# Performance work log

Measured on AMD Instinct MI355X. Metric: run time of the kernel, lower is better.

The kernel has to match this reference:

```python
import jax, jax.numpy as jnp
import numpy as np

EPS = 1e-5

def layer_norm(x, g, b):
    mu = jnp.mean(x, axis=-1, keepdims=True)
    var = jnp.mean(jnp.square(x - mu), axis=-1, keepdims=True)
    return (x - mu) * jax.lax.rsqrt(var + EPS) * g + b

def setup_inputs() -> dict:
    key = jax.random.key(0)
    ks = jax.random.split(key, 12)
    I, H, N = 512, 512, 65536
    s = 0.02
    return {
        "x": jax.random.normal(ks[0], (I,), dtype=jnp.float32),
        "hiddens": jax.random.normal(ks[1], (N, H), dtype=jnp.float32),
        "Wz": jax.random.normal(ks[2], (H, I + H), dtype=jnp.float32) * s,
        "Wri": jax.random.normal(ks[3], (H, I), dtype=jnp.float32) * s,
        "Wrh": jax.random.normal(ks[4], (H, H), dtype=jnp.float32) * s,
        "Wu": jax.random.normal(ks[5], (H, I + H), dtype=jnp.float32) * s,
        "gz": jnp.ones((H,), jnp.float32), "bz": jnp.zeros((H,), jnp.float32),
        "gr": jnp.ones((H,), jnp.float32), "br": jnp.zeros((H,), jnp.float32),
        "gu": jnp.ones((H,), jnp.float32), "bu": jnp.zeros((H,), jnp.float32),
    }

def reference(x, hiddens, Wz, Wri, Wrh, Wu, gz, bz, gr, br, gu, bu):
    # hiddens: [N, H] stacked child hidden states; x: [I]
    hidden_sum = hiddens.sum(0)  # [H]
    # r gate: per-child linear + LayerNorm + sigmoid -> [N, H]
    r_pre = x @ Wri.T + hiddens @ Wrh.T  # broadcast input term over children
    r = jax.nn.sigmoid(layer_norm(r_pre, gr, br))
    # z gate over (input, sum of child hiddens)
    z = jax.nn.sigmoid(layer_norm(jnp.concatenate([x, hidden_sum]) @ Wz.T, gz, bz))
    # candidate with reset-gated child sum
    u = jnp.tanh(layer_norm(jnp.concatenate([x, (r * hiddens).sum(0)]) @ Wu.T, gu, bu))
    h = z * hidden_sum + (1.0 - z) * u
    return h
```

## Files before the change

kernel.cpp:

```cpp
#include <hip/hip_runtime.h>

#define HDIM 512
#define BM 128

typedef __attribute__((ext_vector_type(8))) short bf16x8;
typedef __attribute__((ext_vector_type(4))) float f32x4;

__device__ __forceinline__ unsigned short f2bf(float f){
  union { float f; unsigned int u; } c; c.f = f;
  unsigned int u = c.u;
  unsigned int r = u + 0x7fffu + ((u >> 16) & 1u);
  return (unsigned short)(r >> 16);
}
__device__ __forceinline__ float bf2f(unsigned short b){
  union { unsigned int u; float f; } c; c.u = ((unsigned int)b) << 16;
  return c.f;
}
__device__ __forceinline__ unsigned int pack_trunc(float a, float b){
  return __builtin_amdgcn_perm(__float_as_uint(b), __float_as_uint(a), 0x07060302u);
}
template<int CTRL>
__device__ __forceinline__ float dpp_add(float x){
  int y = __builtin_amdgcn_update_dpp(0, __float_as_int(x), CTRL, 0xf, 0xf, true);
  return x + __int_as_float(y);
}
__device__ __forceinline__ float row_sum16(float x){
  x = dpp_add<0xB1>(x);
  x = dpp_add<0x4E>(x);
  x = dpp_add<0x124>(x);
  x = dpp_add<0x128>(x);
  return x;
}

__global__ __launch_bounds__(256) void prep_k(const float* __restrict__ Wrh,
    unsigned short* __restrict__ wpack, const float* __restrict__ Wri,
    const float* __restrict__ x, float* __restrict__ xwri)
{
  int b = blockIdx.x;
  if (b < 128){
    int t    = b * 256 + threadIdx.x;
    int lane = t & 63;
    int g    = t >> 6;
    int ni   = g & 3;
    int kkk  = (g >> 2) & 15;
    int wc   = g >> 6;
    int row  = wc * 64 + ni * 16 + (lane & 15);
    int k0   = kkk * 32 + (lane >> 4) * 8;
    const float* src = Wrh + (size_t)row * HDIM + k0;
    float4 f0 = *(const float4*)(src);
    float4 f1 = *(const float4*)(src + 4);
    bf16x8 v;
    v[0]=(short)f2bf(f0.x); v[1]=(short)f2bf(f0.y); v[2]=(short)f2bf(f0.z); v[3]=(short)f2bf(f0.w);
    v[4]=(short)f2bf(f1.x); v[5]=(short)f2bf(f1.y); v[6]=(short)f2bf(f1.z); v[7]=(short)f2bf(f1.w);
    *(bf16x8*)(wpack + (size_t)t * 8) = v;
  } else {
    int lane = threadIdx.x & 63, wid = threadIdx.x >> 6;
    int row = (b - 128) * 4 + wid;
    const float* Wr = Wri + (size_t)row * HDIM;
    float a = 0.f;
    #pragma unroll
    for (int k = 0; k < HDIM / 64; k++) a += x[k*64 + lane] * Wr[k*64 + lane];
    #pragma unroll
    for (int m = 1; m < 64; m <<= 1) a += __shfl_xor(a, m, 64);
    if (lane == 0) xwri[row] = a;
  }
}

__global__ __launch_bounds__(1024, 4) void fused_r(
    const float* __restrict__ hiddens,
    const unsigned short* __restrict__ wpack,
    const float* __restrict__ xWri,
    const float* __restrict__ gr, const float* __restrict__ br,
    float* __restrict__ psum_rh, float* __restrict__ psum_h)
{
  __shared__ short As[BM * HDIM];
  __shared__ float redS[8 * 128];
  __shared__ float redQ[8 * 128];
  __shared__ float mu_s[128], rs_s[128];

  const int tid    = threadIdx.x;
  const int lane   = tid & 63;
  const int wid    = tid >> 6;
  const int rowgrp = wid >> 3;
  const int colgrp = wid & 7;
  const int llo    = lane & 15;
  const int lhi    = lane >> 4;
  const int wcol   = colgrp * 64;
  const int rbase  = rowgrp * 64;
  const int r0     = blockIdx.x * BM;

  const int srow = tid >> 3;
  const int scs  = tid & 7;
  const float* aglob = hiddens + (size_t)(r0 + srow) * HDIM + scs * 8;
  char* const wptr = (char*)As + srow * 128 + ((scs * 16) ^ ((srow & 7) << 4));

  const int rdoff = (rbase + llo) * 128 + ((lhi * 16) ^ ((llo & 7) << 4));

  f32x4 acc[4][4];
  #pragma unroll
  for (int i = 0; i < 4; i++)
    #pragma unroll
    for (int j = 0; j < 4; j++)
      #pragma unroll
      for (int k = 0; k < 4; k++) acc[i][j][k] = 0.f;

  const bf16x8* wp = (const bf16x8*)wpack + ((size_t)colgrp * 64) * 64 + lane;
  {
    float4 f0 = *(const float4*)(aglob);
    float4 f1 = *(const float4*)(aglob + 4);
    uint4 w;
    w.x = pack_trunc(f0.x, f0.y); w.y = pack_trunc(f0.z, f0.w);
    w.z = pack_trunc(f1.x, f1.y); w.w = pack_trunc(f1.z, f1.w);
    *(uint4*)(wptr) = w;
  }
  float4 pA0 = *(const float4*)(aglob + 64);
  float4 pA1 = *(const float4*)(aglob + 68);
  asm volatile("s_waitcnt lgkmcnt(0)" ::: "memory");
  __builtin_amdgcn_s_barrier();

  #pragma unroll 1
  for (int p = 0; p < 8; p++){
    const int pb = p * 16384;
    bf16x8 bfr[4];
    #pragma unroll
    for (int ni = 0; ni < 4; ni++) bfr[ni] = wp[(2 * p) * 256 + ni * 64];
    bf16x8 af[4];
    #pragma unroll
    for (int mi = 0; mi < 4; mi++)
      af[mi] = *(const bf16x8*)((char*)As + (pb + rdoff + mi * 2048));
    if (p < 7){
      uint4 w;
      w.x = pack_trunc(pA0.x, pA0.y); w.y = pack_trunc(pA0.z, pA0.w);
      w.z = pack_trunc(pA1.x, pA1.y); w.w = pack_trunc(pA1.z, pA1.w);
      *(uint4*)(wptr + (p + 1) * 16384) = w;
    }
    if (p < 6){
      pA0 = *(const float4*)(aglob + (p + 2) * 64);
      pA1 = *(const float4*)(aglob + (p + 2) * 64 + 4);
    }
    __builtin_amdgcn_s_setprio(1);
    #pragma unroll
    for (int mi = 0; mi < 4; mi++)
      #pragma unroll
      for (int ni = 0; ni < 4; ni++)
        acc[mi][ni] = __builtin_amdgcn_mfma_f32_16x16x32_bf16(af[mi], bfr[ni], acc[mi][ni], 0, 0, 0);
    __builtin_amdgcn_s_setprio(0);
    #pragma unroll
    for (int ni = 0; ni < 4; ni++) bfr[ni] = wp[(2 * p + 1) * 256 + ni * 64];
    #pragma unroll
    for (int mi = 0; mi < 4; mi++)
      af[mi] = *(const bf16x8*)((char*)As + ((pb + rdoff + mi * 2048) ^ 64));
    __builtin_amdgcn_s_setprio(1);
    #pragma unroll
    for (int mi = 0; mi < 4; mi++)
      #pragma unroll
      for (int ni = 0; ni < 4; ni++)
        acc[mi][ni] = __builtin_amdgcn_mfma_f32_16x16x32_bf16(af[mi], bfr[ni], acc[mi][ni], 0, 0, 0);
    __builtin_amdgcn_s_setprio(0);
    asm volatile("s_waitcnt lgkmcnt(0)" ::: "memory");
    __builtin_amdgcn_s_barrier();
  }

  float xw[4], g4[4], b4[4];
  #pragma unroll
  for (int ni = 0; ni < 4; ni++){
    int c = wcol + ni * 16 + llo;
    xw[ni] = xWri[c];
    g4[ni] = gr[c];
    b4[ni] = br[c];
  }
  #pragma unroll
  for (int mi = 0; mi < 4; mi++){
    #pragma unroll
    for (int rr = 0; rr < 4; rr++){
      float sv = 0.f, qv = 0.f;
      #pragma unroll
      for (int ni = 0; ni < 4; ni++){
        float v = acc[mi][ni][rr] + xw[ni];
        acc[mi][ni][rr] = v;
        sv += v; qv += v * v;
      }
      sv = row_sum16(sv);
      qv = row_sum16(qv);
      if (llo == 0){
        int row = rbase + mi * 16 + lhi * 4 + rr;
        redS[colgrp * 128 + row] = sv;
        redQ[colgrp * 128 + row] = qv;
      }
    }
  }
  __syncthreads();
  if (tid < 128){
    float S = 0.f, Q = 0.f;
    #pragma unroll
    for (int w = 0; w < 8; w++){ S += redS[w * 128 + tid]; Q += redQ[w * 128 + tid]; }
    float mu  = S * (1.f / 512.f);
    float var = Q * (1.f / 512.f) - mu * mu;
    mu_s[tid] = mu;
    rs_s[tid] = rsqrtf(var + 1e-5f);
  }
  __syncthreads();

  float prh[4] = {0.f, 0.f, 0.f, 0.f};
  float ph [4] = {0.f, 0.f, 0.f, 0.f};
  #pragma unroll
  for (int mi = 0; mi < 4; mi++){
    #pragma unroll
    for (int rr = 0; rr < 4; rr++){
      int row = rbase + mi * 16 + lhi * 4 + rr;
      float mu = mu_s[row], rs = rs_s[row];
      int sw2 = (row & 7) << 4;
      #pragma unroll
      for (int ni = 0; ni < 4; ni++){
        float v = (acc[mi][ni][rr] - mu) * rs * g4[ni] + b4[ni];
        float r = __builtin_amdgcn_rcpf(1.f + __expf(-v));
        int cb = ni * 32 + llo * 2;
        float h = bf2f(*(const unsigned short*)((char*)As + colgrp * 16384
                     + row * 128 + (cb ^ sw2)));
        prh[ni] += r * h;
        ph [ni] += h;
      }
    }
  }
  #pragma unroll
  for (int ni = 0; ni < 4; ni++){
    prh[ni] += __shfl_xor(prh[ni], 16, 64);
    prh[ni] += __shfl_xor(prh[ni], 32, 64);
    ph [ni] += __shfl_xor(ph [ni], 16, 64);
    ph [ni] += __shfl_xor(ph [ni], 32, 64);
  }
  float* ppRH = redS;
  float* ppH  = redQ;
  if (lhi == 0){
    #pragma unroll
    for (int ni = 0; ni < 4; ni++){
      int col = wcol + ni * 16 + llo;
      ppRH[rowgrp * 512 + col] = prh[ni];
      ppH [rowgrp * 512 + col] = ph[ni];
    }
  }
  __syncthreads();
  if (tid < 512){
    psum_rh[(size_t)blockIdx.x * HDIM + tid] = ppRH[tid] + ppRH[512 + tid];
    psum_h [(size_t)blockIdx.x * HDIM + tid] = ppH[tid]  + ppH[512 + tid];
  }
}

__global__ __launch_bounds__(256) void reduce_psums(
    const float* __restrict__ psum_rh, const float* __restrict__ psum_h,
    const float* __restrict__ x, float* __restrict__ catz, float* __restrict__ catu,
    int nblk)
{
  __shared__ float L[8][32];
  int b = blockIdx.x, t = threadIdx.x;
  if (b < 32){
    const float* P = (b < 16) ? psum_rh : psum_h;
    int c0 = (b & 15) * 32;
    int wj = t >> 5, ci = t & 31;
    float a = 0.f;
    for (int s = wj; s < nblk; s += 8) a += P[(size_t)s * 512 + c0 + ci];
    L[wj][ci] = a;
    __syncthreads();
    if (t < 32){
      float r = 0.f;
      #pragma unroll
      for (int w = 0; w < 8; w++) r += L[w][t];
      if (b < 16) catu[512 + c0 + t] = r;
      else        catz[512 + c0 + t] = r;
    }
  } else {
    int i = ((b - 32) & 1) * 256 + t;
    if (b < 34) catz[i] = x[i];
    else        catu[i] = x[i];
  }
}

__global__ __launch_bounds__(256) void matvec_zu(
    const float* __restrict__ Wz, const float* __restrict__ Wu,
    const float* __restrict__ catz, const float* __restrict__ catu,
    float* __restrict__ zpre, float* __restrict__ upre)
{
  int b = blockIdx.x, lane = threadIdx.x & 63, wid = threadIdx.x >> 6;
  int row = (b & 127) * 4 + wid;
  const float* W = (b < 128) ? Wz : Wu;
  const float* v = (b < 128) ? catz : catu;
  float*       o = (b < 128) ? zpre : upre;
  const float* Wr = W + (size_t)row * 1024;
  float a = 0.f;
  #pragma unroll
  for (int k = 0; k < 1024 / 64; k++) a += v[k*64 + lane] * Wr[k*64 + lane];
  #pragma unroll
  for (int m = 1; m < 64; m <<= 1) a += __shfl_xor(a, m, 64);
  if (lane == 0) o[row] = a;
}

__global__ __launch_bounds__(512) void finalize_k(
    const float* __restrict__ zpre, const float* __restrict__ upre,
    const float* __restrict__ gz, const float* __restrict__ bz,
    const float* __restrict__ gu, const float* __restrict__ bu,
    const float* __restrict__ catz, float* __restrict__ out)
{
  __shared__ float R[8][4];
  int t = threadIdx.x, lane = t & 63, wid = t >> 6;
  float zp = zpre[t], up = upre[t];
  float zs = zp, zq = zp * zp, us = up, uq = up * up;
  #pragma unroll
  for (int m = 1; m < 64; m <<= 1){
    zs += __shfl_xor(zs, m, 64); zq += __shfl_xor(zq, m, 64);
    us += __shfl_xor(us, m, 64); uq += __shfl_xor(uq, m, 64);
  }
  if (lane == 0){ R[wid][0] = zs; R[wid][1] = zq; R[wid][2] = us; R[wid][3] = uq; }
  __syncthreads();
  float ZS = 0.f, ZQ = 0.f, US = 0.f, UQ = 0.f;
  #pragma unroll
  for (int w = 0; w < 8; w++){ ZS += R[w][0]; ZQ += R[w][1]; US += R[w][2]; UQ += R[w][3]; }
  float zmu = ZS / 512.f, zrs = rsqrtf(ZQ / 512.f - zmu * zmu + 1e-5f);
  float umu = US / 512.f, urs = rsqrtf(UQ / 512.f - umu * umu + 1e-5f);
  float z = 1.f / (1.f + expf(-((zp - zmu) * zrs * gz[t] + bz[t])));
  float u = tanhf((up - umu) * urs * gu[t] + bu[t]);
  float hs = catz[512 + t];
  out[t] = z * hs + (1.f - z) * u;
}

extern "C" void kernel_launch(void* const* d_in, const int* in_sizes, int n_in,
                              void* d_out, int out_size, void* d_ws, size_t ws_size,
                              hipStream_t stream)
{
  const float* x   = (const float*)d_in[0];
  const float* hid = (const float*)d_in[1];
  const float* Wz  = (const float*)d_in[2];
  const float* Wri = (const float*)d_in[3];
  const float* Wrh = (const float*)d_in[4];
  const float* Wu  = (const float*)d_in[5];
  const float* gz  = (const float*)d_in[6];
  const float* bz  = (const float*)d_in[7];
  const float* gr  = (const float*)d_in[8];
  const float* br  = (const float*)d_in[9];
  const float* gu  = (const float*)d_in[10];
  const float* bu  = (const float*)d_in[11];
  (void)n_in; (void)out_size; (void)ws_size;

  const int M    = in_sizes[1] / HDIM;
  const int nblk = M / BM;

  char* ws = (char*)d_ws;
  unsigned short* wpack = (unsigned short*)ws;
  float* xwri    = (float*)(ws + 524288);
  float* psum_rh = (float*)(ws + 526336);
  float* psum_h  = (float*)(ws + 526336 + (size_t)nblk * 2048);
  char*  p2      = ws + 526336 + (size_t)nblk * 4096;
  float* catz    = (float*)p2;
  float* catu    = (float*)(p2 + 4096);
  float* zpre    = (float*)(p2 + 8192);
  float* upre    = (float*)(p2 + 10240);
  float* out     = (float*)d_out;

  hipLaunchKernelGGL(prep_k,       dim3(256),  dim3(256),  0, stream, Wrh, wpack, Wri, x, xwri);
  hipLaunchKernelGGL(fused_r,      dim3(nblk), dim3(1024), 0, stream, hid, wpack, xwri, gr, br, psum_rh, psum_h);
  hipLaunchKernelGGL(reduce_psums, dim3(36),   dim3(256),  0, stream, psum_rh, psum_h, x, catz, catu, nblk);
  hipLaunchKernelGGL(matvec_zu,    dim3(256),  dim3(256),  0, stream, Wz, Wu, catz, catu, zpre, upre);
  hipLaunchKernelGGL(finalize_k,   dim3(1),    dim3(512),  0, stream, zpre, upre, gz, bz, gu, bu, catz, out);
}
```

Baseline: 89.70 us.

## Give each wave all 128 rows by 32 columns instead of a 64x64 tile

```diff
diff --git a/kernel.cpp b/kernel.cpp
--- a/kernel.cpp
+++ b/kernel.cpp
@@ -41,11 +41,11 @@
     int t    = b * 256 + threadIdx.x;
     int lane = t & 63;
     int g    = t >> 6;
-    int ni   = g & 3;
-    int kkk  = (g >> 2) & 15;
-    int wc   = g >> 6;
-    int row  = wc * 64 + ni * 16 + (lane & 15);
-    int k0   = kkk * 32 + (lane >> 4) * 8;
+    int ni   = g & 1;
+    int ks   = (g >> 1) & 15;
+    int wc   = g >> 5;
+    int row  = wc * 32 + ni * 16 + (lane & 15);
+    int k0   = ks * 32 + (lane >> 4) * 8;
     const float* src = Wrh + (size_t)row * HDIM + k0;
     float4 f0 = *(const float4*)(src);
     float4 f1 = *(const float4*)(src + 4);
@@ -74,19 +74,16 @@
     float* __restrict__ psum_rh, float* __restrict__ psum_h)
 {
   __shared__ short As[BM * HDIM];
-  __shared__ float redS[8 * 128];
-  __shared__ float redQ[8 * 128];
+  __shared__ float redS[16 * 128];
+  __shared__ float redQ[16 * 128];
   __shared__ float mu_s[128], rs_s[128];
 
   const int tid    = threadIdx.x;
   const int lane   = tid & 63;
-  const int wid    = tid >> 6;
-  const int rowgrp = wid >> 3;
-  const int colgrp = wid & 7;
+  const int colgrp = tid >> 6;
   const int llo    = lane & 15;
   const int lhi    = lane >> 4;
-  const int wcol   = colgrp * 64;
-  const int rbase  = rowgrp * 64;
+  const int wcol   = colgrp * 32;
   const int r0     = blockIdx.x * BM;
 
   const int srow = tid >> 3;
@@ -94,17 +91,17 @@
   const float* aglob = hiddens + (size_t)(r0 + srow) * HDIM + scs * 8;
   char* const wptr = (char*)As + srow * 128 + ((scs * 16) ^ ((srow & 7) << 4));
 
-  const int rdoff = (rbase + llo) * 128 + ((lhi * 16) ^ ((llo & 7) << 4));
-
-  f32x4 acc[4][4];
-  #pragma unroll
-  for (int i = 0; i < 4; i++)
-    #pragma unroll
-    for (int j = 0; j < 4; j++)
+  const int rdoff = llo * 128 + ((lhi * 16) ^ ((llo & 7) << 4));
+
+  f32x4 acc[8][2];
+  #pragma unroll
+  for (int i = 0; i < 8; i++)
+    #pragma unroll
+    for (int j = 0; j < 2; j++)
       #pragma unroll
       for (int k = 0; k < 4; k++) acc[i][j][k] = 0.f;
 
-  const bf16x8* wp = (const bf16x8*)wpack + ((size_t)colgrp * 64) * 64 + lane;
+  const bf16x8* wp = (const bf16x8*)wpack + ((size_t)colgrp * 32) * 64 + lane;
   {
     float4 f0 = *(const float4*)(aglob);
     float4 f1 = *(const float4*)(aglob + 4);
@@ -121,13 +118,6 @@
   #pragma unroll 1
   for (int p = 0; p < 8; p++){
     const int pb = p * 16384;
-    bf16x8 bfr[4];
-    #pragma unroll
-    for (int ni = 0; ni < 4; ni++) bfr[ni] = wp[(2 * p) * 256 + ni * 64];
-    bf16x8 af[4];
-    #pragma unroll
-    for (int mi = 0; mi < 4; mi++)
-      af[mi] = *(const bf16x8*)((char*)As + (pb + rdoff + mi * 2048));
     if (p < 7){
       uint4 w;
       w.x = pack_trunc(pA0.x, pA0.y); w.y = pack_trunc(pA0.z, pA0.w);
@@ -138,52 +128,59 @@
       pA0 = *(const float4*)(aglob + (p + 2) * 64);
       pA1 = *(const float4*)(aglob + (p + 2) * 64 + 4);
     }
-    __builtin_amdgcn_s_setprio(1);
-    #pragma unroll
-    for (int mi = 0; mi < 4; mi++)
-      #pragma unroll
-      for (int ni = 0; ni < 4; ni++)
-        acc[mi][ni] = __builtin_amdgcn_mfma_f32_16x16x32_bf16(af[mi], bfr[ni], acc[mi][ni], 0, 0, 0);
-    __builtin_amdgcn_s_setprio(0);
-    #pragma unroll
-    for (int ni = 0; ni < 4; ni++) bfr[ni] = wp[(2 * p + 1) * 256 + ni * 64];
-    #pragma unroll
-    for (int mi = 0; mi < 4; mi++)
-      af[mi] = *(const bf16x8*)((char*)As + ((pb + rdoff + mi * 2048) ^ 64));
-    __builtin_amdgcn_s_setprio(1);
-    #pragma unroll
-    for (int mi = 0; mi < 4; mi++)
-      #pragma unroll
-      for (int ni = 0; ni < 4; ni++)
-        acc[mi][ni] = __builtin_amdgcn_mfma_f32_16x16x32_bf16(af[mi], bfr[ni], acc[mi][ni], 0, 0, 0);
-    __builtin_amdgcn_s_setprio(0);
+    #pragma unroll
+    for (int kk = 0; kk < 2; kk++){
+      const int ksl = 2 * p + kk;
+      const int xo  = kk ? 64 : 0;
+      bf16x8 bfr[2];
+      #pragma unroll
+      for (int ni = 0; ni < 2; ni++) bfr[ni] = wp[(2 * ksl + ni) * 64];
+      bf16x8 af[4];
+      #pragma unroll
+      for (int mi = 0; mi < 4; mi++)
+        af[mi] = *(const bf16x8*)((char*)As + ((pb + rdoff + mi * 2048) ^ xo));
+      __builtin_amdgcn_s_setprio(1);
+      #pragma unroll
+      for (int mi = 0; mi < 4; mi++)
+        #pragma unroll
+        for (int ni = 0; ni < 2; ni++)
+          acc[mi][ni] = __builtin_amdgcn_mfma_f32_16x16x32_bf16(af[mi], bfr[ni], acc[mi][ni], 0, 0, 0);
+      __builtin_amdgcn_s_setprio(0);
+      #pragma unroll
+      for (int mi = 0; mi < 4; mi++)
+        af[mi] = *(const bf16x8*)((char*)As + ((pb + rdoff + (mi + 4) * 2048) ^ xo));
+      __builtin_amdgcn_s_setprio(1);
+      #pragma unroll
+      for (int mi = 0; mi < 4; mi++)
+        #pragma unroll
+        for (int ni = 0; ni < 2; ni++)
+          acc[mi + 4][ni] = __builtin_amdgcn_mfma_f32_16x16x32_bf16(af[mi], bfr[ni], acc[mi + 4][ni], 0, 0, 0);
+      __builtin_amdgcn_s_setprio(0);
+    }
     asm volatile("s_waitcnt lgkmcnt(0)" ::: "memory");
     __builtin_amdgcn_s_barrier();
   }
 
-  float xw[4], g4[4], b4[4];
-  #pragma unroll
-  for (int ni = 0; ni < 4; ni++){
+  float xw[2], g4[2], b4[2];
+  #pragma unroll
+  for (int ni = 0; ni < 2; ni++){
     int c = wcol + ni * 16 + llo;
     xw[ni] = xWri[c];
     g4[ni] = gr[c];
     b4[ni] = br[c];
   }
   #pragma unroll
-  for (int mi = 0; mi < 4; mi++){
+  for (int mi = 0; mi < 8; mi++){
     #pragma unroll
     for (int rr = 0; rr < 4; rr++){
-      float sv = 0.f, qv = 0.f;
-      #pragma unroll
-      for (int ni = 0; ni < 4; ni++){
-        float v = acc[mi][ni][rr] + xw[ni];
-        acc[mi][ni][rr] = v;
-        sv += v; qv += v * v;
-      }
-      sv = row_sum16(sv);
-      qv = row_sum16(qv);
+      float v0 = acc[mi][0][rr] + xw[0];
+      float v1 = acc[mi][1][rr] + xw[1];
+      acc[mi][0][rr] = v0;
+      acc[mi][1][rr] = v1;
+      float sv = row_sum16(v0 + v1);
+      float qv = row_sum16(v0 * v0 + v1 * v1);
       if (llo == 0){
-        int row = rbase + mi * 16 + lhi * 4 + rr;
+        int row = mi * 16 + lhi * 4 + rr;
         redS[colgrp * 128 + row] = sv;
         redQ[colgrp * 128 + row] = qv;
       }
@@ -193,7 +190,7 @@
   if (tid < 128){
     float S = 0.f, Q = 0.f;
     #pragma unroll
-    for (int w = 0; w < 8; w++){ S += redS[w * 128 + tid]; Q += redQ[w * 128 + tid]; }
+    for (int w = 0; w < 16; w++){ S += redS[w * 128 + tid]; Q += redQ[w * 128 + tid]; }
     float mu  = S * (1.f / 512.f);
     float var = Q * (1.f / 512.f) - mu * mu;
     mu_s[tid] = mu;
@@ -201,21 +198,23 @@
   }
   __syncthreads();
 
-  float prh[4] = {0.f, 0.f, 0.f, 0.f};
-  float ph [4] = {0.f, 0.f, 0.f, 0.f};
-  #pragma unroll
-  for (int mi = 0; mi < 4; mi++){
+  float prh[2] = {0.f, 0.f};
+  float ph [2] = {0.f, 0.f};
+  #pragma unroll
+  for (int mi = 0; mi < 8; mi++){
     #pragma unroll
     for (int rr = 0; rr < 4; rr++){
-      int row = rbase + mi * 16 + lhi * 4 + rr;
+      int row = mi * 16 + lhi * 4 + rr;
       float mu = mu_s[row], rs = rs_s[row];
       int sw2 = (row & 7) << 4;
       #pragma unroll
-      for (int ni = 0; ni < 4; ni++){
+      for (int ni = 0; ni < 2; ni++){
         float v = (acc[mi][ni][rr] - mu) * rs * g4[ni] + b4[ni];
         float r = __builtin_amdgcn_rcpf(1.f + __expf(-v));
-        int cb = ni * 32 + llo * 2;
-        float h = bf2f(*(const unsigned short*)((char*)As + colgrp * 16384
+        int col = wcol + ni * 16 + llo;
+        int pi  = col >> 6;
+        int cb  = (col & 63) * 2;
+        float h = bf2f(*(const unsigned short*)((char*)As + pi * 16384
                      + row * 128 + (cb ^ sw2)));
         prh[ni] += r * h;
         ph [ni] += h;
@@ -223,26 +222,19 @@
     }
   }
   #pragma unroll
-  for (int ni = 0; ni < 4; ni++){
+  for (int ni = 0; ni < 2; ni++){
     prh[ni] += __shfl_xor(prh[ni], 16, 64);
     prh[ni] += __shfl_xor(prh[ni], 32, 64);
     ph [ni] += __shfl_xor(ph [ni], 16, 64);
     ph [ni] += __shfl_xor(ph [ni], 32, 64);
   }
-  float* ppRH = redS;
-  float* ppH  = redQ;
   if (lhi == 0){
     #pragma unroll
-    for (int ni = 0; ni < 4; ni++){
+    for (int ni = 0; ni < 2; ni++){
       int col = wcol + ni * 16 + llo;
-      ppRH[rowgrp * 512 + col] = prh[ni];
-      ppH [rowgrp * 512 + col] = ph[ni];
-    }
-  }
-  __syncthreads();
-  if (tid < 512){
-    psum_rh[(size_t)blockIdx.x * HDIM + tid] = ppRH[tid] + ppRH[512 + tid];
-    psum_h [(size_t)blockIdx.x * HDIM + tid] = ppH[tid]  + ppH[512 + tid];
+      psum_rh[(size_t)blockIdx.x * HDIM + col] = prh[ni];
+      psum_h [(size_t)blockIdx.x * HDIM + col] = ph[ni];
+    }
   }
 }
 
```

After: 91.10 us. About the same (+1.6%).
